# Performance work log

Hardware: AMD Instinct MI355X
Metric: run time of the kernel (lower is better)

The kernel has to match this reference:

```python
import jax, jax.numpy as jnp
import numpy as np

NUM_HEADS = 20


def _rope(t, pos):
    """Rotary embedding (ESM style, rotate_half on full head_dim).
    t: (T, h, d), pos: (T,) float32 position within each sequence."""
    d = t.shape[-1]
    inv_freq = 1.0 / (10000.0 ** (jnp.arange(0, d, 2, dtype=jnp.float32) / d))  # (d/2,)
    freqs = pos[:, None] * inv_freq[None, :]          # (T, d/2)
    emb = jnp.concatenate([freqs, freqs], axis=-1)    # (T, d)
    cos = jnp.cos(emb)[:, None, :]                    # (T, 1, d)
    sin = jnp.sin(emb)[:, None, :]
    x1, x2 = jnp.split(t, 2, axis=-1)
    rot = jnp.concatenate([-x2, x1], axis=-1)
    return t * cos + rot * sin


def setup_inputs() -> dict:
    key = jax.random.key(0)
    ks = jax.random.split(key, 8)
    E = 1280
    lengths = np.array([512, 768, 1024, 1024, 1024, 1280, 1280, 1280], dtype=np.int64)
    cu_lens = jnp.asarray(np.concatenate([[0], np.cumsum(lengths)]).astype(np.int32))
    T = int(lengths.sum())  # 8192
    s = (2.0 / (E + E)) ** 0.5  # xavier-ish scale
    return {
        "x": jax.random.normal(ks[0], (T, E), jnp.float32),
        "cu_lens": cu_lens,
        "max_len": 1280,
        "Wq": jax.random.normal(ks[1], (E, E), jnp.float32) * s,
        "bq": jnp.zeros((E,), jnp.float32),
        "Wk": jax.random.normal(ks[2], (E, E), jnp.float32) * s,
        "bk": jnp.zeros((E,), jnp.float32),
        "Wv": jax.random.normal(ks[3], (E, E), jnp.float32) * s,
        "bv": jnp.zeros((E,), jnp.float32),
        "Wo": jax.random.normal(ks[4], (E, E), jnp.float32) * (2.0 ** 0.5) * s,
        "bo": jnp.zeros((E,), jnp.float32),
    }


def reference(x, cu_lens, max_len, Wq, bq, Wk, bk, Wv, bv, Wo, bo):
    T, E = x.shape
    h = NUM_HEADS
    d = E // h
    scale = d ** -0.5
    # fused QKV projections (q pre-scaled, softmax_scale=1 as in the original)
    q = ((x @ Wq.T + bq) * scale).reshape(T, h, d)
    k = (x @ Wk.T + bk).reshape(T, h, d)
    v = (x @ Wv.T + bv).reshape(T, h, d)
    # per-token sequence id and within-sequence position from cu_lens
    t_idx = jnp.arange(T)
    seq_id = jnp.searchsorted(cu_lens, t_idx, side='right') - 1  # (T,)
    pos = t_idx - cu_lens[seq_id]                                # (T,) int
    # rotary on q and k with per-sequence positions
    posf = pos.astype(jnp.float32)
    q = _rope(q, posf)
    k = _rope(k, posf)
    # scatter packed tokens into padded (B, max_len, h, d) layout
    B = cu_lens.shape[0] - 1
    qp = jnp.zeros((B, max_len, h, d), q.dtype).at[seq_id, pos].set(q)
    kp = jnp.zeros((B, max_len, h, d), k.dtype).at[seq_id, pos].set(k)
    vp = jnp.zeros((B, max_len, h, d), v.dtype).at[seq_id, pos].set(v)
    valid = jnp.zeros((B, max_len), bool).at[seq_id, pos].set(True)
    # non-causal attention within each sequence (block-diagonal over packed tokens)
    scores = jnp.einsum('blhd,bmhd->bhlm', qp, kp)
    scores = jnp.where(valid[:, None, None, :], scores, -1e9)
    attn = jax.nn.softmax(scores, axis=-1)
    o = jnp.einsum('bhlm,bmhd->blhd', attn, vp)
    # gather back to packed layout and apply output projection
    out_tok = o[seq_id, pos].reshape(T, E)
    return out_tok @ Wo.T + bo
```

## Files before the change

### kernel.cpp

```cpp
#include <hip/hip_runtime.h>
#include <hip/hip_bf16.h>
#include <cstdint>

#define E_DIM   1280
#define NHEADS  20
#define HDIM    64
#define QKV_LD  3840

typedef __attribute__((ext_vector_type(8))) short bf8_t;
typedef __attribute__((ext_vector_type(4))) short bf4_t;
typedef __attribute__((ext_vector_type(4))) float f4_t;

__device__ __forceinline__ short f2bs(float f) {
    union { __hip_bfloat16 h; short s; } u;
    u.h = __float2bfloat16(f);
    return u.s;
}

__device__ __forceinline__ f4_t mfma16x32(bf8_t a, bf8_t b, f4_t c) {
    return __builtin_amdgcn_mfma_f32_16x16x32_bf16(a, b, c, 0, 0, 0);
}
__device__ __forceinline__ f4_t mfma16x16(bf4_t a, bf4_t b, f4_t c) {
    return __builtin_amdgcn_mfma_f32_16x16x16bf16_1k(a, b, c, 0, 0, 0);
}

__device__ __forceinline__ void gl_lds16(const void* g, void* l) {
    auto gp = reinterpret_cast<__attribute__((address_space(1))) unsigned int*>(
        reinterpret_cast<uintptr_t>(g));
    auto lp = reinterpret_cast<__attribute__((address_space(3))) unsigned int*>(
        reinterpret_cast<uintptr_t>(l));
    __builtin_amdgcn_global_load_lds(gp, lp, 16, 0, 0);
}

#define QSCALE 0.18033688011112042f

__device__ __forceinline__ void cvt8(__hip_bfloat16* dst, const float* src, float sc) {
    float4 a = *(const float4*)src;
    float4 b = *(const float4*)(src + 4);
    bf8_t v;
    v[0] = f2bs(a.x * sc); v[1] = f2bs(a.y * sc); v[2] = f2bs(a.z * sc); v[3] = f2bs(a.w * sc);
    v[4] = f2bs(b.x * sc); v[5] = f2bs(b.y * sc); v[6] = f2bs(b.z * sc); v[7] = f2bs(b.w * sc);
    *(bf8_t*)dst = v;
}

__global__ __launch_bounds__(256) void prep_kernel(
    const float* __restrict__ x,
    const float* __restrict__ wq, const float* __restrict__ wk,
    const float* __restrict__ wv, const float* __restrict__ wo,
    const float* __restrict__ bq, const float* __restrict__ bk, const float* __restrict__ bv,
    __hip_bfloat16* __restrict__ xbf, __hip_bfloat16* __restrict__ wqkv,
    __hip_bfloat16* __restrict__ wobf, float* __restrict__ bqkv,
    long nx8, long nw8, long nb8)
{
    long u = (long)blockIdx.x * 256 + threadIdx.x;
    if (u < nx8) { cvt8(xbf + u * 8, x + u * 8, 1.0f); return; }
    u -= nx8;
    if (u < 3 * nw8) {
        long e = u * 8;
        long w1 = nw8 * 8;
        const float* src; float sc;
        if (e < w1)            { src = wq + e;           sc = QSCALE; }
        else if (e < 2 * w1)   { src = wk + (e - w1);    sc = 1.0f; }
        else                   { src = wv + (e - 2*w1);  sc = 1.0f; }
        cvt8(wqkv + e, src, sc);
        return;
    }
    u -= 3 * nw8;
    if (u < nw8) { cvt8(wobf + u * 8, wo + u * 8, 1.0f); return; }
    u -= nw8;
    if (u < nb8) {
        long e = u * 8;
        #pragma unroll
        for (int j = 0; j < 8; j++) {
            long i = e + j;
            float v;
            if (i < E_DIM)           v = bq[i] * QSCALE;
            else if (i < 2 * E_DIM)  v = bk[i - E_DIM];
            else                     v = bv[i - 2 * E_DIM];
            bqkv[i] = v;
        }
    }
}

template<bool BF16_OUT>
__global__ __launch_bounds__(256, 3) void gemm_nt(
    const __hip_bfloat16* __restrict__ A, const __hip_bfloat16* __restrict__ Bw,
    const float* __restrict__ bias, void* __restrict__ Cout,
    int M, int N, int K, int ldc)
{
    __shared__ __align__(16) __hip_bfloat16 As[128 * 32];
    __shared__ __align__(16) __hip_bfloat16 Bs[128 * 32];
    const int t = threadIdx.x;
    const int wv = t >> 6;
    const int ln = t & 63;
    const int m16 = ln & 15, q4 = ln >> 4;
    const int row0 = blockIdx.y * 128, col0 = blockIdx.x * 128;
    const int wm = (wv >> 1) * 64, wn = (wv & 1) * 64;

    f4_t acc[4][4] = {};

    for (int k0 = 0; k0 < K; k0 += 32) {
        #pragma unroll
        for (int i = 0; i < 2; i++) {
            int s = i * 256 + t;
            int r = s >> 2, c = s & 3;
            gl_lds16(A + (size_t)(row0 + r) * K + k0 + c * 8,
                     As + (size_t)(i * 256 + wv * 64) * 8);
        }
        #pragma unroll
        for (int i = 0; i < 2; i++) {
            int s = i * 256 + t;
            int r = s >> 2, c = s & 3;
            gl_lds16(Bw + (size_t)(col0 + r) * K + k0 + c * 8,
                     Bs + (size_t)(i * 256 + wv * 64) * 8);
        }
        __syncthreads();
        bf8_t af[4], bfr[4];
        #pragma unroll
        for (int mt = 0; mt < 4; mt++)
            af[mt] = *(const bf8_t*)&As[(wm + mt * 16 + m16) * 32 + q4 * 8];
        #pragma unroll
        for (int nt = 0; nt < 4; nt++)
            bfr[nt] = *(const bf8_t*)&Bs[(wn + nt * 16 + m16) * 32 + q4 * 8];
        #pragma unroll
        for (int mt = 0; mt < 4; mt++)
            #pragma unroll
            for (int nt = 0; nt < 4; nt++)
                acc[mt][nt] = mfma16x32(af[mt], bfr[nt], acc[mt][nt]);
        __syncthreads();
    }

    #pragma unroll
    for (int nt = 0; nt < 4; nt++) {
        int cg = col0 + wn + nt * 16 + m16;
        float bv = bias[cg];
        #pragma unroll
        for (int mt = 0; mt < 4; mt++) {
            #pragma unroll
            for (int r = 0; r < 4; r++) {
                int rg = row0 + wm + mt * 16 + q4 * 4 + r;
                float v = acc[mt][nt][r] + bv;
                if constexpr (BF16_OUT)
                    ((__hip_bfloat16*)Cout)[(long)rg * ldc + cg] = __float2bfloat16(v);
                else
                    ((float*)Cout)[(long)rg * ldc + cg] = v;
            }
        }
    }
}

template<bool BF16_OUT>
__global__ __launch_bounds__(512, 2) void gemm256(
    const __hip_bfloat16* __restrict__ A, const __hip_bfloat16* __restrict__ Bw,
    const float* __restrict__ bias, void* __restrict__ Cout,
    int M, int N, int K, int ldc)
{
    __shared__ __align__(16) __hip_bfloat16 As[2][256 * 64];
    __shared__ __align__(16) __hip_bfloat16 Bs[2][256 * 64];

    const int t = threadIdx.x;
    const int wv = t >> 6, ln = t & 63;
    const int m16 = ln & 15, q4 = ln >> 4;
    const int wr = wv >> 2, wc = wv & 3;

    const int gx = N >> 8;
    const int nwg = gridDim.x;
    const int id = blockIdx.x;
    const int swz = ((nwg & 7) == 0) ? (id & 7) * (nwg >> 3) + (id >> 3) : id;
    const int col0 = (swz % gx) << 8;
    const int row0 = (swz / gx) << 8;

    const int NT = K >> 6;

    auto stage = [&](const __hip_bfloat16* src, __hip_bfloat16* dst) {
        #pragma unroll
        for (int i = 0; i < 4; i++) {
            int s = i * 512 + t;
            int r = s >> 3, c = (s & 7) ^ (r & 7);
            gl_lds16(src + (size_t)r * K + c * 8,
                     (char*)dst + (size_t)(i * 512 + wv * 64) * 16);
        }
    };

    stage(A  + (size_t)row0 * K,      &As[0][0]);
    stage(Bw + (size_t)col0 * K,      &Bs[0][0]);
    if (NT > 1) {
        stage(A  + (size_t)row0 * K + 64, &As[1][0]);
        stage(Bw + (size_t)col0 * K + 64, &Bs[1][0]);
        asm volatile("s_waitcnt vmcnt(8)" ::: "memory");
    } else {
        asm volatile("s_waitcnt vmcnt(0)" ::: "memory");
    }
    __builtin_amdgcn_s_barrier();

    f4_t acc[8][4] = {};

    for (int kt = 0; kt < NT; kt++) {
        const __hip_bfloat16* Ab = &As[kt & 1][0];
        const __hip_bfloat16* Bb = &Bs[kt & 1][0];

        auto lda = [&](const __hip_bfloat16* base, int r, int kc) {
            return *(const bf8_t*)&base[r * 64 + ((((kc << 2) | q4) ^ (r & 7)) << 3)];
        };

        bf8_t afr[4][2], bf0[2][2], bf1[2][2];
        #pragma unroll
        for (int mt = 0; mt < 4; mt++)
            #pragma unroll
            for (int kc = 0; kc < 2; kc++)
                afr[mt][kc] = lda(Ab, wr * 128 + mt * 16 + m16, kc);
        #pragma unroll
        for (int nt = 0; nt < 2; nt++)
            #pragma unroll
            for (int kc = 0; kc < 2; kc++)
                bf0[nt][kc] = lda(Bb, wc * 64 + nt * 16 + m16, kc);

        __builtin_amdgcn_s_setprio(1);
        #pragma unroll
        for (int mt = 0; mt < 4; mt++)
            #pragma unroll
            for (int nt = 0; nt < 2; nt++)
                #pragma unroll
                for (int kc = 0; kc < 2; kc++)
                    acc[mt][nt] = mfma16x32(afr[mt][kc], bf0[nt][kc], acc[mt][nt]);
        __builtin_amdgcn_s_setprio(0);

        #pragma unroll
        for (int nt = 0; nt < 2; nt++)
            #pragma unroll
            for (int kc = 0; kc < 2; kc++)
                bf1[nt][kc] = lda(Bb, wc * 64 + (2 + nt) * 16 + m16, kc);

        __builtin_amdgcn_s_setprio(1);
        #pragma unroll
        for (int mt = 0; mt < 4; mt++)
            #pragma unroll
            for (int nt = 0; nt < 2; nt++)
                #pragma unroll
                for (int kc = 0; kc < 2; kc++)
                    acc[mt][2 + nt] = mfma16x32(afr[mt][kc], bf1[nt][kc], acc[mt][2 + nt]);
        __builtin_amdgcn_s_setprio(0);

        #pragma unroll
        for (int mt = 0; mt < 4; mt++)
            #pragma unroll
            for (int kc = 0; kc < 2; kc++)
                afr[mt][kc] = lda(Ab, wr * 128 + (4 + mt) * 16 + m16, kc);

        __builtin_amdgcn_s_setprio(1);
        #pragma unroll
        for (int mt = 0; mt < 4; mt++)
            #pragma unroll
            for (int nt = 0; nt < 2; nt++)
                #pragma unroll
                for (int kc = 0; kc < 2; kc++)
                    acc[4 + mt][2 + nt] = mfma16x32(afr[mt][kc], bf1[nt][kc], acc[4 + mt][2 + nt]);
        __builtin_amdgcn_s_setprio(0);

        __builtin_amdgcn_s_setprio(1);
        #pragma unroll
        for (int mt = 0; mt < 4; mt++)
            #pragma unroll
            for (int nt = 0; nt < 2; nt++)
                #pragma unroll
                for (int kc = 0; kc < 2; kc++)
                    acc[4 + mt][nt] = mfma16x32(afr[mt][kc], bf0[nt][kc], acc[4 + mt][nt]);
        __builtin_amdgcn_s_setprio(0);

        asm volatile("s_waitcnt lgkmcnt(0)" ::: "memory");
        __builtin_amdgcn_s_barrier();

        if (kt + 2 < NT) {
            stage(A  + (size_t)row0 * K + (size_t)(kt + 2) * 64, &As[kt & 1][0]);
            stage(Bw + (size_t)col0 * K + (size_t)(kt + 2) * 64, &Bs[kt & 1][0]);
        }
        if (kt + 1 < NT) {
            if (kt + 2 < NT)
                asm volatile("s_waitcnt vmcnt(8)" ::: "memory");
            else
                asm volatile("s_waitcnt vmcnt(0)" ::: "memory");
            __builtin_amdgcn_s_barrier();
        }
    }

    #pragma unroll
    for (int nt = 0; nt < 4; nt++) {
        int cg = col0 + wc * 64 + nt * 16 + m16;
        float bval = bias[cg];
        #pragma unroll
        for (int mt = 0; mt < 8; mt++) {
            #pragma unroll
            for (int r = 0; r < 4; r++) {
                int rg = row0 + wr * 128 + mt * 16 + q4 * 4 + r;
                float v = acc[mt][nt][r] + bval;
                if constexpr (BF16_OUT)
                    ((__hip_bfloat16*)Cout)[(long)rg * ldc + cg] = __float2bfloat16(v);
                else
                    ((float*)Cout)[(long)rg * ldc + cg] = v;
            }
        }
    }
}

__global__ __launch_bounds__(256) void rope_kernel(
    __hip_bfloat16* __restrict__ qkv, const int* __restrict__ cu, int B, int T)
{
    long idx = (long)blockIdx.x * 256 + threadIdx.x;
    int i = idx & 31;
    long r = idx >> 5;
    int h = (int)(r % NHEADS);
    int tok = (int)(r / NHEADS);
    if (tok >= T) return;
    int pos = tok;
    for (int b = 1; b <= B; b++) if (tok >= cu[b]) pos = tok - cu[b];
    float f = (float)pos * exp2f(-(float)i * 0.41524100558003436f);
    float s, c;
    sincosf(f, &s, &c);
    long base = (long)tok * QKV_LD + h * HDIM + i;
    {
        float q1 = __bfloat162float(qkv[base]);
        float q2 = __bfloat162float(qkv[base + 32]);
        qkv[base]      = __float2bfloat16(q1 * c - q2 * s);
        qkv[base + 32] = __float2bfloat16(q2 * c + q1 * s);
    }
    {
        long kb = base + E_DIM;
        float k1 = __bfloat162float(qkv[kb]);
        float k2 = __bfloat162float(qkv[kb + 32]);
        qkv[kb]      = __float2bfloat16(k1 * c - k2 * s);
        qkv[kb + 32] = __float2bfloat16(k2 * c + k1 * s);
    }
}

__global__ __launch_bounds__(256) void vtrans_kernel(
    const __hip_bfloat16* __restrict__ qkv, __hip_bfloat16* __restrict__ vt, int T)
{
    long u = (long)blockIdx.x * 256 + threadIdx.x;
    int tchunks = T >> 3;
    int tc = (int)(u % tchunks);
    int hd = (int)(u / tchunks);
    if (hd >= E_DIM) return;
    long t0 = (long)tc * 8;
    bf8_t v;
    #pragma unroll
    for (int j = 0; j < 8; j++)
        v[j] = *(const short*)&qkv[(t0 + j) * QKV_LD + 2 * E_DIM + hd];
    *(bf8_t*)&vt[(long)hd * T + t0] = v;
}

__global__ __launch_bounds__(256, 2) void attn_kernel(
    const __hip_bfloat16* __restrict__ qkv, const __hip_bfloat16* __restrict__ vt,
    const int* __restrict__ cu, __hip_bfloat16* __restrict__ obuf, int B, int T)
{
    __shared__ __align__(16) __hip_bfloat16 Ks[2][128 * 64];
    __shared__ __align__(16) __hip_bfloat16 Vs[2][64 * 128];

    int idx = blockIdx.x;
    int h = idx % NHEADS;
    int gt = idx / NHEADS;
    int b = 0, l = 0, seq0 = 0;
    for (; b < B; ++b) {
        seq0 = cu[b];
        l = cu[b + 1] - seq0;
        int ntile = (l + 127) >> 7;
        if (gt < ntile) break;
        gt -= ntile;
    }
    if (b == B) return;
    int q0 = gt * 128;

    const int t = threadIdx.x;
    const int wv = t >> 6, ln = t & 63;
    const int m16 = ln & 15, q4 = ln >> 4;

    auto stage_full = [&](int kv0n, int bi) {
        #pragma unroll
        for (int i = 0; i < 4; i++) {
            int s2 = i * 256 + t;
            int key = s2 >> 3, cg = (s2 & 7) ^ (key & 7);
            gl_lds16(qkv + (long)(seq0 + kv0n + key) * QKV_LD + E_DIM + h * HDIM + cg * 8,
                     (char*)&Ks[bi][0] + (size_t)(i * 256 + wv * 64) * 16);
        }
        #pragma unroll
        for (int i = 0; i < 4; i++) {
            int s2 = i * 256 + t;
            int d = s2 >> 4, cg = (s2 & 15) ^ (d & 15);
            gl_lds16(vt + (long)(h * HDIM + d) * T + seq0 + kv0n + cg * 8,
                     (char*)&Vs[bi][0] + (size_t)(i * 256 + wv * 64) * 16);
        }
    };
    auto stage_tail = [&](int kv0n, int bi) {
        #pragma unroll
        for (int i = 0; i < 4; i++) {
            int s2 = i * 256 + t;
            int key = s2 >> 3, c = s2 & 7;
            bf8_t v = (bf8_t)0;
            if (kv0n + key < l)
                v = *(const bf8_t*)(qkv + (long)(seq0 + kv0n + key) * QKV_LD + E_DIM + h * HDIM + c * 8);
            *(bf8_t*)&Ks[bi][key * 64 + (c ^ (key & 7)) * 8] = v;
        }
        #pragma unroll
        for (int i = 0; i < 4; i++) {
            int s2 = i * 256 + t;
            int d = s2 >> 4, c = s2 & 15;
            bf8_t v = (bf8_t)0;
            int tb = kv0n + c * 8;
            #pragma unroll
            for (int u = 0; u < 8; u++)
                if (tb + u < l)
                    v[u] = *(const short*)&vt[(long)(h * HDIM + d) * T + seq0 + tb + u];
            *(bf8_t*)&Vs[bi][d * 128 + (c ^ (d & 15)) * 8] = v;
        }
    };

    if (128 <= l) stage_full(0, 0); else stage_tail(0, 0);

    bf8_t bq[2][2];
    #pragma unroll
    for (int nt = 0; nt < 2; nt++) {
        int qrow = q0 + wv * 32 + nt * 16 + m16;
        #pragma unroll
        for (int kc = 0; kc < 2; kc++) {
            bf8_t v = (bf8_t)0;
            if (qrow < l)
                v = *(const bf8_t*)(qkv + (long)(seq0 + qrow) * QKV_LD + h * HDIM + kc * 32 + q4 * 8);
            bq[nt][kc] = v;
        }
    }

    f4_t oacc[2][4] = {};
    float m_s[2] = {-1e30f, -1e30f};
    float l_s[2] = {0.0f, 0.0f};

    const int ksw0 = (q4 ^ (m16 & 7)) * 8;
    const int ksw1 = ((4 + q4) ^ (m16 & 7)) * 8;

    asm volatile("s_waitcnt vmcnt(0) lgkmcnt(0)" ::: "memory");
    __builtin_amdgcn_s_barrier();

    int cur = 0;
    for (int kv0 = 0; kv0 < l; kv0 += 128) {
        const bool full = (kv0 + 128 <= l);
        const int kvn = kv0 + 128;
        const bool has_next = kvn < l;
        if (has_next) {
            if (kvn + 128 <= l) stage_full(kvn, cur ^ 1);
            else stage_tail(kvn, cur ^ 1);
        }

        const __hip_bfloat16* Kb = Ks[cur];
        const __hip_bfloat16* Vb = Vs[cur];

        f4_t S[2][8];
        __builtin_amdgcn_s_setprio(1);
        #pragma unroll
        for (int mt = 0; mt < 8; mt++) {
            const __hip_bfloat16* krow = &Kb[(mt * 16 + m16) * 64];
            bf8_t ak0 = *(const bf8_t*)(krow + ksw0);
            bf8_t ak1 = *(const bf8_t*)(krow + ksw1);
            #pragma unroll
            for (int nt = 0; nt < 2; nt++) {
                f4_t a = {};
                a = mfma16x32(ak0, bq[nt][0], a);
                a = mfma16x32(ak1, bq[nt][1], a);
                S[nt][mt] = a;
            }
        }
        __builtin_amdgcn_s_setprio(0);

        if (!full) {
            #pragma unroll
            for (int mt = 0; mt < 8; mt++) {
                #pragma unroll
                for (int r = 0; r < 4; r++) {
                    bool valid = (kv0 + mt * 16 + q4 * 4 + r) < l;
                    #pragma unroll
                    for (int nt = 0; nt < 2; nt++)
                        if (!valid) S[nt][mt][r] = -1e30f;
                }
            }
        }

        #pragma unroll
        for (int nt = 0; nt < 2; nt++) {
            float mx = -1e30f;
            #pragma unroll
            for (int mt = 0; mt < 8; mt++)
                #pragma unroll
                for (int r = 0; r < 4; r++)
                    mx = fmaxf(mx, S[nt][mt][r]);
            mx = fmaxf(mx, __shfl_xor(mx, 16));
            mx = fmaxf(mx, __shfl_xor(mx, 32));
            if (!__all(mx - m_s[nt] <= 8.0f)) {
                float mn = fmaxf(m_s[nt], mx);
                float al = exp2f(m_s[nt] - mn);
                m_s[nt] = mn;
                l_s[nt] *= al;
                #pragma unroll
                for (int dt = 0; dt < 4; dt++)
                    #pragma unroll
                    for (int r = 0; r < 4; r++)
                        oacc[nt][dt][r] *= al;
            }
            float mcur = m_s[nt];
            float ls = 0.0f;
            #pragma unroll
            for (int mt = 0; mt < 8; mt++) {
                #pragma unroll
                for (int r = 0; r < 4; r++) {
                    float p = exp2f(S[nt][mt][r] - mcur);
                    ls += p;
                    S[nt][mt][r] = p;
                }
            }
            l_s[nt] += ls;
        }

        __builtin_amdgcn_s_setprio(1);
        #pragma unroll
        for (int mt = 0; mt < 8; mt++) {
            bf4_t bp[2];
            #pragma unroll
            for (int nt = 0; nt < 2; nt++) {
                bf4_t p;
                p[0] = f2bs(S[nt][mt][0]); p[1] = f2bs(S[nt][mt][1]);
                p[2] = f2bs(S[nt][mt][2]); p[3] = f2bs(S[nt][mt][3]);
                bp[nt] = p;
            }
            const int vsw = ((mt * 2 + (q4 >> 1)) ^ m16) * 8 + (q4 & 1) * 4;
            #pragma unroll
            for (int dt = 0; dt < 4; dt++) {
                bf4_t av = *(const bf4_t*)&Vb[(dt * 16 + m16) * 128 + vsw];
                #pragma unroll
                for (int nt = 0; nt < 2; nt++)
                    oacc[nt][dt] = mfma16x16(av, bp[nt], oacc[nt][dt]);
            }
        }
        __builtin_amdgcn_s_setprio(0);

        if (has_next) {
            asm volatile("s_waitcnt vmcnt(0) lgkmcnt(0)" ::: "memory");
            __builtin_amdgcn_s_barrier();
            cur ^= 1;
        }
    }

    #pragma unroll
    for (int nt = 0; nt < 2; nt++) {
        float ls = l_s[nt];
        ls += __shfl_xor(ls, 16);
        ls += __shfl_xor(ls, 32);
        float inv = 1.0f / ls;
        int qrow = q0 + wv * 32 + nt * 16 + m16;
        if (qrow < l) {
            #pragma unroll
            for (int dt = 0; dt < 4; dt++) {
                bf4_t o;
                #pragma unroll
                for (int r = 0; r < 4; r++)
                    o[r] = f2bs(oacc[nt][dt][r] * inv);
                *(bf4_t*)&obuf[(long)(seq0 + qrow) * E_DIM + h * HDIM + dt * 16 + q4 * 4] = o;
            }
        }
    }
}

extern "C" void kernel_launch(void* const* d_in, const int* in_sizes, int n_in,
                              void* d_out, int out_size, void* d_ws, size_t ws_size,
                              hipStream_t stream) {
    const int E = E_DIM;
    const int T = in_sizes[0] / E;
    const int B = in_sizes[1] - 1;

    const float* x  = (const float*)d_in[0];
    const int*   cu = (const int*)d_in[1];
    const float* Wq = (const float*)d_in[3];
    const float* bq = (const float*)d_in[4];
    const float* Wk = (const float*)d_in[5];
    const float* bk = (const float*)d_in[6];
    const float* Wv = (const float*)d_in[7];
    const float* bv = (const float*)d_in[8];
    const float* Wo = (const float*)d_in[9];
    const float* bo = (const float*)d_in[10];

    char* ws = (char*)d_ws;
    size_t off = 0;
    auto alloc = [&](size_t bytes) -> void* {
        void* p = ws + off;
        off = (off + bytes + 255) & ~(size_t)255;
        return p;
    };
    __hip_bfloat16* xbf   = (__hip_bfloat16*)alloc((size_t)T * E * 2);
    __hip_bfloat16* wqkv  = (__hip_bfloat16*)alloc((size_t)3 * E * E * 2);
    __hip_bfloat16* wobf  = (__hip_bfloat16*)alloc((size_t)E * E * 2);
    float*          bqkv  = (float*)alloc((size_t)3 * E * 4);
    __hip_bfloat16* qkvb  = (__hip_bfloat16*)alloc((size_t)T * 3 * E * 2);
    __hip_bfloat16* vt    = (__hip_bfloat16*)alloc((size_t)E * T * 2);
    __hip_bfloat16* obuf  = xbf;

    long nx8 = (long)T * E / 8;
    long nw8 = (long)E * E / 8;
    long nb8 = (long)3 * E / 8;
    long total = nx8 + 4 * nw8 + nb8;
    int pblocks = (int)((total + 255) / 256);
    prep_kernel<<<pblocks, 256, 0, stream>>>(x, Wq, Wk, Wv, Wo, bq, bk, bv,
                                             xbf, wqkv, wobf, bqkv, nx8, nw8, nb8);

    gemm256<true><<<(T / 256) * (3 * E / 256), 512, 0, stream>>>(
        xbf, wqkv, bqkv, qkvb, T, 3 * E, E, 3 * E);

    rope_kernel<<<(int)(((long)T * NHEADS * 32) / 256), 256, 0, stream>>>(qkvb, cu, B, T);

    vtrans_kernel<<<(int)(((long)E * T / 8 + 255) / 256), 256, 0, stream>>>(qkvb, vt, T);

    int qtiles_ub = T / 128 + B;
    attn_kernel<<<qtiles_ub * NHEADS, 256, 0, stream>>>(qkvb, vt, cu, obuf, B, T);

    gemm_nt<false><<<dim3(E / 128, T / 128), 256, 0, stream>>>(
        obuf, wobf, bo, d_out, T, E, E, E);
}
```

Before: 428.0 us.

## Fuse V transpose into QKV GEMM epilogue and software-pipeline attention PV

The QKV GEMM epilogue now writes the V columns directly in transposed layout, which removes the separate vtrans kernel and its strided global reads. The attention loop is software-pipelined: the P·V MFMAs for the previous KV tile run after the QK^T of the current tile, with a triple-buffered V tile in LDS. bf16 packing now uses v_cvt_pk_bf16_f32. The extra V buffer raises LDS use and the held P registers raise register pressure, which may reduce occupancy.

```diff
diff --git a/kernel.cpp b/kernel.cpp
--- a/kernel.cpp
+++ b/kernel.cpp
@@ -15,6 +15,13 @@
     union { __hip_bfloat16 h; short s; } u;
     u.h = __float2bfloat16(f);
     return u.s;
+}
+
+__device__ __forceinline__ bf4_t pk4(f4_t s) {
+    union { bf4_t v; uint32_t u[2]; } r;
+    asm("v_cvt_pk_bf16_f32 %0, %1, %2" : "=v"(r.u[0]) : "v"(s[0]), "v"(s[1]));
+    asm("v_cvt_pk_bf16_f32 %0, %1, %2" : "=v"(r.u[1]) : "v"(s[2]), "v"(s[3]));
+    return r.v;
 }
 
 __device__ __forceinline__ f4_t mfma16x32(bf8_t a, bf8_t b, f4_t c) {
@@ -149,10 +156,10 @@
     }
 }
 
-template<bool BF16_OUT>
 __global__ __launch_bounds__(512, 2) void gemm256(
     const __hip_bfloat16* __restrict__ A, const __hip_bfloat16* __restrict__ Bw,
-    const float* __restrict__ bias, void* __restrict__ Cout,
+    const float* __restrict__ bias, __hip_bfloat16* __restrict__ Cout,
+    __hip_bfloat16* __restrict__ vtout, int Tdim,
     int M, int N, int K, int ldc)
 {
     __shared__ __align__(16) __hip_bfloat16 As[2][256 * 64];
@@ -283,20 +290,33 @@
         }
     }
 
-    #pragma unroll
-    for (int nt = 0; nt < 4; nt++) {
-        int cg = col0 + wc * 64 + nt * 16 + m16;
-        float bval = bias[cg];
-        #pragma unroll
-        for (int mt = 0; mt < 8; mt++) {
-            #pragma unroll
-            for (int r = 0; r < 4; r++) {
-                int rg = row0 + wr * 128 + mt * 16 + q4 * 4 + r;
-                float v = acc[mt][nt][r] + bval;
-                if constexpr (BF16_OUT)
-                    ((__hip_bfloat16*)Cout)[(long)rg * ldc + cg] = __float2bfloat16(v);
-                else
-                    ((float*)Cout)[(long)rg * ldc + cg] = v;
+    if (col0 >= 2 * E_DIM) {
+        #pragma unroll
+        for (int nt = 0; nt < 4; nt++) {
+            int cg = col0 + wc * 64 + nt * 16 + m16;
+            float bval = bias[cg];
+            int vrow = cg - 2 * E_DIM;
+            #pragma unroll
+            for (int mt = 0; mt < 8; mt++) {
+                int rg0 = row0 + wr * 128 + mt * 16 + q4 * 4;
+                f4_t vv;
+                #pragma unroll
+                for (int r = 0; r < 4; r++) vv[r] = acc[mt][nt][r] + bval;
+                *(bf4_t*)&vtout[(long)vrow * Tdim + rg0] = pk4(vv);
+            }
+        }
+    } else {
+        #pragma unroll
+        for (int nt = 0; nt < 4; nt++) {
+            int cg = col0 + wc * 64 + nt * 16 + m16;
+            float bval = bias[cg];
+            #pragma unroll
+            for (int mt = 0; mt < 8; mt++) {
+                #pragma unroll
+                for (int r = 0; r < 4; r++) {
+                    int rg = row0 + wr * 128 + mt * 16 + q4 * 4 + r;
+                    Cout[(long)rg * ldc + cg] = __float2bfloat16(acc[mt][nt][r] + bval);
+                }
             }
         }
     }
@@ -332,28 +352,12 @@
     }
 }
 
-__global__ __launch_bounds__(256) void vtrans_kernel(
-    const __hip_bfloat16* __restrict__ qkv, __hip_bfloat16* __restrict__ vt, int T)
-{
-    long u = (long)blockIdx.x * 256 + threadIdx.x;
-    int tchunks = T >> 3;
-    int tc = (int)(u % tchunks);
-    int hd = (int)(u / tchunks);
-    if (hd >= E_DIM) return;
-    long t0 = (long)tc * 8;
-    bf8_t v;
-    #pragma unroll
-    for (int j = 0; j < 8; j++)
-        v[j] = *(const short*)&qkv[(t0 + j) * QKV_LD + 2 * E_DIM + hd];
-    *(bf8_t*)&vt[(long)hd * T + t0] = v;
-}
-
 __global__ __launch_bounds__(256, 2) void attn_kernel(
     const __hip_bfloat16* __restrict__ qkv, const __hip_bfloat16* __restrict__ vt,
     const int* __restrict__ cu, __hip_bfloat16* __restrict__ obuf, int B, int T)
 {
     __shared__ __align__(16) __hip_bfloat16 Ks[2][128 * 64];
-    __shared__ __align__(16) __hip_bfloat16 Vs[2][64 * 128];
+    __shared__ __align__(16) __hip_bfloat16 Vs[3][64 * 128];
 
     int idx = blockIdx.x;
     int h = idx % NHEADS;
@@ -368,28 +372,29 @@
     }
     if (b == B) return;
     int q0 = gt * 128;
+    const int NT = (l + 127) >> 7;
 
     const int t = threadIdx.x;
     const int wv = t >> 6, ln = t & 63;
     const int m16 = ln & 15, q4 = ln >> 4;
 
-    auto stage_full = [&](int kv0n, int bi) {
+    auto stage_full = [&](int kv0n, int kb, int vb) {
         #pragma unroll
         for (int i = 0; i < 4; i++) {
             int s2 = i * 256 + t;
             int key = s2 >> 3, cg = (s2 & 7) ^ (key & 7);
             gl_lds16(qkv + (long)(seq0 + kv0n + key) * QKV_LD + E_DIM + h * HDIM + cg * 8,
-                     (char*)&Ks[bi][0] + (size_t)(i * 256 + wv * 64) * 16);
+                     (char*)&Ks[kb][0] + (size_t)(i * 256 + wv * 64) * 16);
         }
         #pragma unroll
         for (int i = 0; i < 4; i++) {
             int s2 = i * 256 + t;
             int d = s2 >> 4, cg = (s2 & 15) ^ (d & 15);
             gl_lds16(vt + (long)(h * HDIM + d) * T + seq0 + kv0n + cg * 8,
-                     (char*)&Vs[bi][0] + (size_t)(i * 256 + wv * 64) * 16);
+                     (char*)&Vs[vb][0] + (size_t)(i * 256 + wv * 64) * 16);
         }
     };
-    auto stage_tail = [&](int kv0n, int bi) {
+    auto stage_tail = [&](int kv0n, int kb, int vb) {
         #pragma unroll
         for (int i = 0; i < 4; i++) {
             int s2 = i * 256 + t;
@@ -397,7 +402,7 @@
             bf8_t v = (bf8_t)0;
             if (kv0n + key < l)
                 v = *(const bf8_t*)(qkv + (long)(seq0 + kv0n + key) * QKV_LD + E_DIM + h * HDIM + c * 8);
-            *(bf8_t*)&Ks[bi][key * 64 + (c ^ (key & 7)) * 8] = v;
+            *(bf8_t*)&Ks[kb][key * 64 + (c ^ (key & 7)) * 8] = v;
         }
         #pragma unroll
         for (int i = 0; i < 4; i++) {
@@ -409,11 +414,11 @@
             for (int u = 0; u < 8; u++)
                 if (tb + u < l)
                     v[u] = *(const short*)&vt[(long)(h * HDIM + d) * T + seq0 + tb + u];
-            *(bf8_t*)&Vs[bi][d * 128 + (c ^ (d & 15)) * 8] = v;
+            *(bf8_t*)&Vs[vb][d * 128 + (c ^ (d & 15)) * 8] = v;
         }
     };
 
-    if (128 <= l) stage_full(0, 0); else stage_tail(0, 0);
+    if (128 <= l) stage_full(0, 0, 0); else stage_tail(0, 0, 0);
 
     bf8_t bq[2][2];
     #pragma unroll
@@ -431,25 +436,40 @@
     f4_t oacc[2][4] = {};
     float m_s[2] = {-1e30f, -1e30f};
     float l_s[2] = {0.0f, 0.0f};
+    bf4_t bp[8][2];
+    int vprev = 0;
 
     const int ksw0 = (q4 ^ (m16 & 7)) * 8;
     const int ksw1 = ((4 + q4) ^ (m16 & 7)) * 8;
 
+    auto do_pv = [&](const __hip_bfloat16* Vb) {
+        __builtin_amdgcn_s_setprio(1);
+        #pragma unroll
+        for (int mt = 0; mt < 8; mt++) {
+            const int vsw = ((mt * 2 + (q4 >> 1)) ^ m16) * 8 + (q4 & 1) * 4;
+            #pragma unroll
+            for (int dt = 0; dt < 4; dt++) {
+                bf4_t av = *(const bf4_t*)&Vb[(dt * 16 + m16) * 128 + vsw];
+                #pragma unroll
+                for (int nt = 0; nt < 2; nt++)
+                    oacc[nt][dt] = mfma16x16(av, bp[mt][nt], oacc[nt][dt]);
+            }
+        }
+        __builtin_amdgcn_s_setprio(0);
+    };
+
     asm volatile("s_waitcnt vmcnt(0) lgkmcnt(0)" ::: "memory");
     __builtin_amdgcn_s_barrier();
 
-    int cur = 0;
-    for (int kv0 = 0; kv0 < l; kv0 += 128) {
+    for (int it = 0; it < NT; ++it) {
+        const int kv0 = it << 7;
         const bool full = (kv0 + 128 <= l);
-        const int kvn = kv0 + 128;
-        const bool has_next = kvn < l;
-        if (has_next) {
-            if (kvn + 128 <= l) stage_full(kvn, cur ^ 1);
-            else stage_tail(kvn, cur ^ 1);
-        }
-
-        const __hip_bfloat16* Kb = Ks[cur];
-        const __hip_bfloat16* Vb = Vs[cur];
+        if (it + 1 < NT) {
+            int kvn = kv0 + 128;
+            if (kvn + 128 <= l) stage_full(kvn, (it + 1) & 1, (it + 1) % 3);
+            else stage_tail(kvn, (it + 1) & 1, (it + 1) % 3);
+        }
+        const __hip_bfloat16* Kb = Ks[it & 1];
 
         f4_t S[2][8];
         __builtin_amdgcn_s_setprio(1);
@@ -480,6 +500,8 @@
                 }
             }
         }
+
+        if (it > 0) do_pv(Vs[vprev]);
 
         #pragma unroll
         for (int nt = 0; nt < 2; nt++) {
@@ -516,34 +538,20 @@
             l_s[nt] += ls;
         }
 
-        __builtin_amdgcn_s_setprio(1);
-        #pragma unroll
-        for (int mt = 0; mt < 8; mt++) {
-            bf4_t bp[2];
-            #pragma unroll
-            for (int nt = 0; nt < 2; nt++) {
-                bf4_t p;
-                p[0] = f2bs(S[nt][mt][0]); p[1] = f2bs(S[nt][mt][1]);
-                p[2] = f2bs(S[nt][mt][2]); p[3] = f2bs(S[nt][mt][3]);
-                bp[nt] = p;
-            }
-            const int vsw = ((mt * 2 + (q4 >> 1)) ^ m16) * 8 + (q4 & 1) * 4;
-            #pragma unroll
-            for (int dt = 0; dt < 4; dt++) {
-                bf4_t av = *(const bf4_t*)&Vb[(dt * 16 + m16) * 128 + vsw];
-                #pragma unroll
-                for (int nt = 0; nt < 2; nt++)
-                    oacc[nt][dt] = mfma16x16(av, bp[nt], oacc[nt][dt]);
-            }
-        }
-        __builtin_amdgcn_s_setprio(0);
-
-        if (has_next) {
+        #pragma unroll
+        for (int mt = 0; mt < 8; mt++)
+            #pragma unroll
+            for (int nt = 0; nt < 2; nt++)
+                bp[mt][nt] = pk4(S[nt][mt]);
+        vprev = it % 3;
+
+        if (it + 1 < NT) {
             asm volatile("s_waitcnt vmcnt(0) lgkmcnt(0)" ::: "memory");
             __builtin_amdgcn_s_barrier();
-            cur ^= 1;
-        }
-    }
+        }
+    }
+
+    do_pv(Vs[vprev]);
 
     #pragma unroll
     for (int nt = 0; nt < 2; nt++) {
@@ -555,11 +563,11 @@
         if (qrow < l) {
             #pragma unroll
             for (int dt = 0; dt < 4; dt++) {
-                bf4_t o;
+                f4_t o;
                 #pragma unroll
                 for (int r = 0; r < 4; r++)
-                    o[r] = f2bs(oacc[nt][dt][r] * inv);
-                *(bf4_t*)&obuf[(long)(seq0 + qrow) * E_DIM + h * HDIM + dt * 16 + q4 * 4] = o;
+                    o[r] = oacc[nt][dt][r] * inv;
+                *(bf4_t*)&obuf[(long)(seq0 + qrow) * E_DIM + h * HDIM + dt * 16 + q4 * 4] = pk4(o);
             }
         }
     }
@@ -606,12 +614,10 @@
     prep_kernel<<<pblocks, 256, 0, stream>>>(x, Wq, Wk, Wv, Wo, bq, bk, bv,
                                              xbf, wqkv, wobf, bqkv, nx8, nw8, nb8);
 
-    gemm256<true><<<(T / 256) * (3 * E / 256), 512, 0, stream>>>(
-        xbf, wqkv, bqkv, qkvb, T, 3 * E, E, 3 * E);
+    gemm256<<<(T / 256) * (3 * E / 256), 512, 0, stream>>>(
+        xbf, wqkv, bqkv, qkvb, vt, T, T, 3 * E, E, 3 * E);
 
     rope_kernel<<<(int)(((long)T * NHEADS * 32) / 256), 256, 0, stream>>>(qkvb, cu, B, T);
-
-    vtrans_kernel<<<(int)(((long)E * T / 8 + 255) / 256), 256, 0, stream>>>(qkvb, vt, T);
 
     int qtiles_ub = T / 128 + B;
     attn_kernel<<<qtiles_ub * NHEADS, 256, 0, stream>>>(qkvb, vt, cu, obuf, B, T);
```

Result: faster. 385.9 us (-9.9%).
